# Kernel tuning notes

Hardware: AMD Instinct MI355X
Metric: run time of the kernel (lower is better)

Reference implementation:

```python
import jax, jax.numpy as jnp
import numpy as np

DF = 2  # downsampling_factor

def _conv1x1(x, w, b):
    # x: [N,C,T,H,W], w: [O,C], b: [O]
    return jnp.einsum('ncthw,oc->nothw', x, w) + b[None, :, None, None, None]

def _avgpool(x):
    # AvgPool3d(kernel=(1,k,k), stride=(1,s,s), pad=(0,p,p)), count_include_pad=True
    k, s = DF + 1, DF
    p = (DF + 1) // 2
    summed = jax.lax.reduce_window(
        x, 0.0, jax.lax.add,
        window_dimensions=(1, 1, 1, k, k),
        window_strides=(1, 1, 1, s, s),
        padding=((0, 0), (0, 0), (0, 0), (p, p), (p, p)))
    return summed / float(k * k)

def _grid(T, Hd, Wd, t_scale):
    xg = jnp.arange(Wd, dtype=jnp.float32) / ((Wd - 1) * 0.25) - 2.0
    yg = jnp.arange(Hd, dtype=jnp.float32) / ((Hd - 1) * 0.5) - 1.0
    tg = (jnp.arange(T, dtype=jnp.float32) / ((T - 1) * 0.5) - 1.0) * t_scale
    return jnp.stack(jnp.meshgrid(tg, yg, xg, indexing='ij'), axis=0)  # [3,T,Hd,Wd]

def setup_inputs() -> dict:
    key = jax.random.key(0)
    ks = jax.random.split(key, 9)
    C, IC, OC = 256, 128, 256
    x = jax.random.normal(ks[0], (2, C, 4, 64, 64), dtype=jnp.float32)
    sc = 0.05
    return {
        'x': x,
        'theta_w': jax.random.normal(ks[1], (IC, C), jnp.float32) * sc,
        'theta_b': jax.random.normal(ks[2], (IC,), jnp.float32) * sc,
        'phi_w': jax.random.normal(ks[3], (IC, C), jnp.float32) * sc,
        'phi_b': jax.random.normal(ks[4], (IC,), jnp.float32) * sc,
        'g_w': jax.random.normal(ks[5], (IC, C), jnp.float32) * sc,
        'g_b': jax.random.normal(ks[6], (IC,), jnp.float32) * sc,
        'W_w': jax.random.normal(ks[7], (OC, IC + 3), jnp.float32) * sc,
        'W_b': jax.random.normal(ks[8], (OC,), jnp.float32) * sc,
    }

def reference(x, theta_w, theta_b, phi_w, phi_b, g_w, g_b, W_w, W_b):
    N, C, T, H, W = x.shape
    IC = theta_w.shape[0]
    theta_x = _conv1x1(x, theta_w, theta_b)                       # [N,IC,T,H,W]
    theta_x = theta_x.transpose(0, 2, 3, 4, 1).reshape(N, T * H * W, IC)
    phi_x = _avgpool(_conv1x1(x, phi_w, phi_b))                   # [N,IC,T,Hd,Wd]
    Hd, Wd = phi_x.shape[-2], phi_x.shape[-1]
    phi_x = phi_x.reshape(N, IC, T * Hd * Wd)
    f_x = jax.nn.softmax(jnp.matmul(theta_x, phi_x), axis=-1)     # [N,THW,THdWd]
    g_x = _avgpool(_conv1x1(x, g_w, g_b))                         # [N,IC,T,Hd,Wd]
    grid = _grid(T, Hd, Wd, 0.1)                                   # [3,T,Hd,Wd]
    g_x = jnp.concatenate(
        [g_x, jnp.broadcast_to(grid[None], (N, 3, T, Hd, Wd))], axis=1)
    g_x = g_x.transpose(0, 2, 3, 4, 1).reshape(N, T * Hd * Wd, IC + 3)
    y = jnp.matmul(f_x, g_x)                                       # [N,THW,IC+3]
    y = y.transpose(0, 2, 1).reshape(N, IC + 3, T, H, W)
    return _conv1x1(y, W_w, W_b)
```

## Files before the change

### kernel.cpp

```cpp
#include <hip/hip_runtime.h>
#include <stdint.h>

typedef short short8 __attribute__((ext_vector_type(8)));
typedef float floatx4 __attribute__((ext_vector_type(4)));
typedef float floatx16 __attribute__((ext_vector_type(16)));
typedef unsigned uint4v __attribute__((ext_vector_type(4)));

#define MFMA16(a, b, c) __builtin_amdgcn_mfma_f32_16x16x32_bf16((a), (b), (c), 0, 0, 0)
#define MFMA32(a, b, c) __builtin_amdgcn_mfma_f32_32x32x16_bf16((a), (b), (c), 0, 0, 0)

__device__ __forceinline__ unsigned short f2bf(float f) {
    union { float f; unsigned u; } v; v.f = f;
    unsigned u = v.u;
    unsigned r = (u + 0x7FFFu + ((u >> 16) & 1u)) >> 16;
    return (unsigned short)r;
}
__device__ __forceinline__ unsigned pkfast(float lo, float hi) {
    unsigned a = __float_as_uint(lo) + 0x8000u;
    unsigned b = __float_as_uint(hi) + 0x8000u;
    return __builtin_amdgcn_perm(b, a, 0x07060302u);
}

__global__ void k_prep(const float* th, const float* ph, const float* gw, const float* Ww,
                       unsigned short* TW, unsigned short* PW, unsigned short* GW,
                       unsigned short* Wp) {
    int i = blockIdx.x * 256 + threadIdx.x;
    if (i < 32768) {
        TW[i] = f2bf(th[i]);
    } else if (i < 65536) {
        PW[i - 32768] = f2bf(ph[i - 32768]);
    } else if (i < 98304) {
        GW[i - 65536] = f2bf(gw[i - 65536]);
    } else if (i < 98304 + 256 * 160) {
        int j = i - 98304;
        int oc = j / 160, k = j - oc * 160;
        Wp[j] = (k < 131) ? f2bf(Ww[oc * 131 + k]) : (unsigned short)0;
    }
}

__global__ void k_pool(const float* __restrict__ x, float* __restrict__ xp) {
    int e = blockIdx.x * 256 + threadIdx.x;
    int wd = e & 31, hd = (e >> 5) & 31, t = (e >> 10) & 3, c = (e >> 12) & 255, n = e >> 20;
    const float* base = x + (((size_t)(n * 256 + c) * 4 + t) << 12);
    int h0 = 2 * hd - 1, w0 = 2 * wd - 1;
    float s = 0.f;
    #pragma unroll
    for (int dh = 0; dh < 3; ++dh) {
        int h = h0 + dh;
        if ((unsigned)h < 64u) {
            const float* row = base + h * 64;
            #pragma unroll
            for (int dw = 0; dw < 3; ++dw) {
                int w = w0 + dw;
                if ((unsigned)w < 64u) s += row[w];
            }
        }
    }
    xp[((size_t)(n * 256 + c) << 12) + (t << 10) + (hd << 5) + wd] = s * (1.f / 9.f);
}

__launch_bounds__(256)
__global__ void k_convq(const float* __restrict__ x, const unsigned short* __restrict__ TW,
                        const float* __restrict__ tb, unsigned short* __restrict__ Q) {
    int tid = threadIdx.x, wid = tid >> 6, lane = tid & 63, quad = lane >> 4, l16 = lane & 15;
    int n = blockIdx.y;
    int px = blockIdx.x * 64 + wid * 16 + l16;
    const float* xb = x + ((size_t)n << 22) + px;
    floatx4 acc[8];
    #pragma unroll
    for (int i = 0; i < 8; ++i) acc[i] = (floatx4)0.f;
    for (int kc = 0; kc < 8; ++kc) {
        int cbase = kc * 32 + quad * 8;
        short8 b;
        #pragma unroll
        for (int j = 0; j < 8; ++j) b[j] = (short)f2bf(xb[(size_t)(cbase + j) << 14]);
        #pragma unroll
        for (int mt = 0; mt < 8; ++mt) {
            short8 a = *(const short8*)(TW + (mt * 16 + l16) * 256 + cbase);
            acc[mt] = MFMA16(a, b, acc[mt]);
        }
    }
    unsigned short* Qr = Q + ((((size_t)n << 14) + px) << 7);
    #pragma unroll
    for (int mt = 0; mt < 8; ++mt)
        #pragma unroll
        for (int r = 0; r < 4; ++r) {
            int ic = mt * 16 + quad * 4 + r;
            Qr[ic] = f2bf(acc[mt][r] + tb[ic]);
        }
}

__launch_bounds__(256)
__global__ void k_convkv(const float* __restrict__ xp,
                         const unsigned short* __restrict__ PW, const float* __restrict__ pb,
                         const unsigned short* __restrict__ GW, const float* __restrict__ gb,
                         unsigned short* __restrict__ K, unsigned short* __restrict__ Vt) {
    int tid = threadIdx.x, wid = tid >> 6, lane = tid & 63, quad = lane >> 4, l16 = lane & 15;
    int n = blockIdx.y;
    int k0 = blockIdx.x * 64;
    int key = k0 + wid * 16 + l16;
    const float* xb = xp + ((size_t)n << 20) + key;
    floatx4 ka[8], va[8];
    #pragma unroll
    for (int i = 0; i < 8; ++i) { ka[i] = (floatx4)0.f; va[i] = (floatx4)0.f; }
    for (int kc = 0; kc < 8; ++kc) {
        int cbase = kc * 32 + quad * 8;
        short8 b;
        #pragma unroll
        for (int j = 0; j < 8; ++j) b[j] = (short)f2bf(xb[(size_t)(cbase + j) << 12]);
        #pragma unroll
        for (int mt = 0; mt < 8; ++mt) {
            short8 ap = *(const short8*)(PW + (mt * 16 + l16) * 256 + cbase);
            ka[mt] = MFMA16(ap, b, ka[mt]);
            short8 ag = *(const short8*)(GW + (mt * 16 + l16) * 256 + cbase);
            va[mt] = MFMA16(ag, b, va[mt]);
        }
    }
    int hd = (key >> 5) & 31, wdd = key & 31;
    float frac = ((hd == 0) ? 2.f : 3.f) * ((wdd == 0) ? 2.f : 3.f) * (1.f / 9.f);
    unsigned short* Kr = K + ((((size_t)n << 12) + key) << 7);
    #pragma unroll
    for (int mt = 0; mt < 8; ++mt)
        #pragma unroll
        for (int r = 0; r < 4; ++r) {
            int ic = mt * 16 + quad * 4 + r;
            Kr[ic] = f2bf(ka[mt][r] + pb[ic] * frac);
            Vt[(((size_t)n * 160 + ic) << 12) + key] = f2bf(va[mt][r] + gb[ic] * frac);
        }
    #pragma unroll
    for (int it = 0; it < 8; ++it) {
        int e = it * 256 + tid;
        int row = 128 + (e >> 6);
        int kk = k0 + (e & 63);
        int t = kk >> 10, hh = (kk >> 5) & 31, ww = kk & 31;
        unsigned short v = 0;
        if (row == 128) v = f2bf(((float)t * (1.f / 1.5f) - 1.f) * 0.1f);
        else if (row == 129) v = f2bf((float)hh * (1.f / 15.5f) - 1.f);
        else if (row == 130) v = f2bf((float)ww * (1.f / 7.75f) - 2.f);
        Vt[(((size_t)n * 160 + row) << 12) + kk] = v;
    }
}

__launch_bounds__(256, 2)
__global__ void k_attn(const unsigned short* __restrict__ Q, const unsigned short* __restrict__ K,
                       const unsigned short* __restrict__ Vt, unsigned short* __restrict__ Y,
                       float* __restrict__ L) {
    __shared__ short Klds[64][136];
    __shared__ short Vlds[160][72];
    int tid = threadIdx.x, wid = tid >> 6, lane = tid & 63;
    int l32 = lane & 31, half = lane >> 5;
    int n = blockIdx.y, sp = blockIdx.z;
    int q0 = blockIdx.x * 128 + wid * 32;

    const unsigned short* Qr = Q + ((((size_t)n << 14) + q0 + l32) << 7);
    short8 qf[8];
    #pragma unroll
    for (int kc = 0; kc < 8; ++kc) qf[kc] = *(const short8*)(Qr + kc * 16 + half * 8);

    floatx16 O[5];
    #pragma unroll
    for (int t = 0; t < 5; ++t) O[t] = (floatx16)0.f;
    float lacc = 0.f;

    int krow = tid >> 4, kcol = (tid & 15) * 8;
    int vrow = tid >> 3, vcol = (tid & 7) * 8;
    const unsigned short* kptr = K + ((((size_t)n << 12) + sp * 2048 + krow) << 7) + kcol;
    const unsigned short* vptr = Vt + ((size_t)(n * 160 + vrow) << 12) + sp * 2048 + vcol;

    short8 kpre[4], vpre[5];
    #pragma unroll
    for (int i = 0; i < 4; ++i) kpre[i] = *(const short8*)(kptr + (size_t)i * 16 * 128);
    #pragma unroll
    for (int i = 0; i < 5; ++i) vpre[i] = *(const short8*)(vptr + ((size_t)i * 32 << 12));

    for (int it = 0; it < 32; ++it) {
        __syncthreads();
        #pragma unroll
        for (int i = 0; i < 4; ++i) *(short8*)&Klds[i * 16 + krow][kcol] = kpre[i];
        #pragma unroll
        for (int i = 0; i < 5; ++i) *(short8*)&Vlds[i * 32 + vrow][vcol] = vpre[i];
        __syncthreads();
        if (it < 31) {
            const unsigned short* kp = kptr + (size_t)(it + 1) * 64 * 128;
            const unsigned short* vp = vptr + (size_t)(it + 1) * 64;
            #pragma unroll
            for (int i = 0; i < 4; ++i) kpre[i] = *(const short8*)(kp + (size_t)i * 16 * 128);
            #pragma unroll
            for (int i = 0; i < 5; ++i) vpre[i] = *(const short8*)(vp + ((size_t)i * 32 << 12));
        }

        #pragma unroll
        for (int ks = 0; ks < 2; ++ks) {
            floatx16 st = (floatx16)0.f;
            #pragma unroll
            for (int kc = 0; kc < 8; ++kc) {
                short8 kf = *(const short8*)&Klds[ks * 32 + l32][kc * 16 + half * 8];
                st = MFMA32(kf, qf[kc], st);
            }
            unsigned u[8];
            #pragma unroll
            for (int a = 0; a < 4; ++a) {
                float p0 = exp2f(fmaf(st[4 * a + 0], 1.44269504f, -17.3123404907f));
                float p1 = exp2f(fmaf(st[4 * a + 1], 1.44269504f, -17.3123404907f));
                float p2 = exp2f(fmaf(st[4 * a + 2], 1.44269504f, -17.3123404907f));
                float p3 = exp2f(fmaf(st[4 * a + 3], 1.44269504f, -17.3123404907f));
                lacc += (p0 + p1) + (p2 + p3);
                u[2 * a] = pkfast(p0, p1);
                u[2 * a + 1] = pkfast(p2, p3);
            }
            unsigned xu[8];
            #pragma unroll
            for (int g = 0; g < 8; ++g) xu[g] = (unsigned)__shfl_xor((int)u[g], 32);
            uint4v pw0, pw1;
            pw0[0] = half ? xu[2] : u[0];
            pw0[1] = half ? xu[3] : u[1];
            pw0[2] = half ? u[2] : xu[0];
            pw0[3] = half ? u[3] : xu[1];
            pw1[0] = half ? xu[6] : u[4];
            pw1[1] = half ? xu[7] : u[5];
            pw1[2] = half ? u[6] : xu[4];
            pw1[3] = half ? u[7] : xu[5];
            short8 pf0 = __builtin_bit_cast(short8, pw0);
            short8 pf1 = __builtin_bit_cast(short8, pw1);
            #pragma unroll
            for (int vt = 0; vt < 5; ++vt) {
                short8 vf0 = *(const short8*)&Vlds[vt * 32 + l32][ks * 32 + half * 8];
                O[vt] = MFMA32(vf0, pf0, O[vt]);
                short8 vf1 = *(const short8*)&Vlds[vt * 32 + l32][ks * 32 + 16 + half * 8];
                O[vt] = MFMA32(vf1, pf1, O[vt]);
            }
        }
    }
    float lt = lacc + __shfl_xor(lacc, 32);
    unsigned short* Yb = Y + ((((size_t)(sp * 2 + n) << 14) + q0 + l32) * 160);
    #pragma unroll
    for (int vt = 0; vt < 5; ++vt)
        #pragma unroll
        for (int g = 0; g < 4; ++g) {
            int vd = vt * 32 + 8 * g + 4 * half;
            uint2 w;
            w.x = pkfast(O[vt][4 * g], O[vt][4 * g + 1]);
            w.y = pkfast(O[vt][4 * g + 2], O[vt][4 * g + 3]);
            *(uint2*)(Yb + vd) = w;
        }
    if (lane < 32) L[(((size_t)(sp * 2 + n)) << 14) + q0 + lane] = lt;
}

__launch_bounds__(256)
__global__ void k_convf(const unsigned short* __restrict__ Y, const float* __restrict__ L,
                        const unsigned short* __restrict__ Wp, const float* __restrict__ Wb,
                        float* __restrict__ out) {
    int tid = threadIdx.x, wid = tid >> 6, lane = tid & 63, quad = lane >> 4, l16 = lane & 15;
    int n = blockIdx.y;
    int p0 = blockIdx.x * 64;
    floatx4 acc[4][4];
    #pragma unroll
    for (int i = 0; i < 4; ++i)
        #pragma unroll
        for (int j = 0; j < 4; ++j) acc[i][j] = (floatx4)0.f;
    for (int kc = 0; kc < 5; ++kc) {
        int cb = kc * 32 + quad * 8;
        short8 a[4];
        #pragma unroll
        for (int mt = 0; mt < 4; ++mt)
            a[mt] = *(const short8*)(Wp + (size_t)(wid * 64 + mt * 16 + l16) * 160 + cb);
        #pragma unroll
        for (int sp = 0; sp < 2; ++sp) {
            const unsigned short* Yb = Y + ((((size_t)(sp * 2 + n)) << 14) + p0) * 160;
            #pragma unroll
            for (int nt = 0; nt < 4; ++nt) {
                short8 b = *(const short8*)(Yb + (size_t)(nt * 16 + l16) * 160 + cb);
                #pragma unroll
                for (int mt = 0; mt < 4; ++mt) acc[mt][nt] = MFMA16(a[mt], b, acc[mt][nt]);
            }
        }
    }
    float linv[4];
    #pragma unroll
    for (int nt = 0; nt < 4; ++nt) {
        int p = p0 + nt * 16 + l16;
        linv[nt] = 1.f / (L[(((size_t)n) << 14) + p] + L[(((size_t)(2 + n)) << 14) + p]);
    }
    #pragma unroll
    for (int mt = 0; mt < 4; ++mt)
        #pragma unroll
        for (int r = 0; r < 4; ++r) {
            int oc = wid * 64 + mt * 16 + quad * 4 + r;
            float bb = Wb[oc];
            float* orow = out + ((((size_t)n << 8) + oc) << 14) + p0;
            #pragma unroll
            for (int nt = 0; nt < 4; ++nt)
                orow[nt * 16 + l16] = acc[mt][nt][r] * linv[nt] + bb;
        }
}

extern "C" void kernel_launch(void* const* d_in, const int* in_sizes, int n_in,
                              void* d_out, int out_size, void* d_ws, size_t ws_size,
                              hipStream_t stream) {
    (void)in_sizes; (void)n_in; (void)out_size; (void)ws_size;
    const float* x   = (const float*)d_in[0];
    const float* thw = (const float*)d_in[1];
    const float* thb = (const float*)d_in[2];
    const float* phw = (const float*)d_in[3];
    const float* phb = (const float*)d_in[4];
    const float* gw_ = (const float*)d_in[5];
    const float* gb_ = (const float*)d_in[6];
    const float* Ww  = (const float*)d_in[7];
    const float* Wb  = (const float*)d_in[8];
    float* out = (float*)d_out;

    char* ws = (char*)d_ws;
    size_t off = 0;
    auto alloc = [&](size_t b) { size_t o = off; off += (b + 255) & ~(size_t)255; return o; };
    unsigned short* TW = (unsigned short*)(ws + alloc(32768 * 2));
    unsigned short* PW = (unsigned short*)(ws + alloc(32768 * 2));
    unsigned short* GW = (unsigned short*)(ws + alloc(32768 * 2));
    unsigned short* Wp = (unsigned short*)(ws + alloc(40960 * 2));
    unsigned short* Qb = (unsigned short*)(ws + alloc((size_t)32768 * 128 * 2));
    unsigned short* Kb = (unsigned short*)(ws + alloc((size_t)8192 * 128 * 2));
    unsigned short* Vt = (unsigned short*)(ws + alloc((size_t)2 * 160 * 4096 * 2));
    float*          Lb = (float*)(ws + alloc((size_t)2 * 2 * 16384 * 4));
    unsigned short* Yb = (unsigned short*)(ws + alloc((size_t)2 * 2 * 16384 * 160 * 2));
    float*          xp = (float*)((char*)Yb + (size_t)2 * 16384 * 160 * 2);

    k_prep<<<(139264 + 255) / 256, 256, 0, stream>>>(thw, phw, gw_, Ww, TW, PW, GW, Wp);
    k_pool<<<8192, 256, 0, stream>>>(x, xp);
    k_convq<<<dim3(256, 2), 256, 0, stream>>>(x, TW, thb, Qb);
    k_convkv<<<dim3(64, 2), 256, 0, stream>>>(xp, PW, phb, GW, gb_, Kb, Vt);
    k_attn<<<dim3(128, 2, 2), 256, 0, stream>>>(Qb, Kb, Vt, Yb, Lb);
    k_convf<<<dim3(256, 2), 256, 0, stream>>>(Yb, Lb, Wp, Wb, out);
}
```

Measured before the change: 273.1 us.

## Split attention keys three ways and stage conv outputs through LDS for coalesced stores

The attention kernel now splits the key range into three chunks instead of two, which launches more blocks, and raises the launch-bounds occupancy hint to 3 blocks per SM. The final conv sums over all splits. The Q, K and Vt conv kernels now stage their bf16 results in shared memory and write them out as wide vector stores instead of scattered 16-bit stores. They also use a packed fast bf16 conversion instead of per-element rounding. The extra split adds Y partial traffic, and the higher occupancy target can force register spills in the attention kernel.

```diff
diff --git a/kernel.cpp b/kernel.cpp
--- a/kernel.cpp
+++ b/kernel.cpp
@@ -8,6 +8,8 @@
 
 #define MFMA16(a, b, c) __builtin_amdgcn_mfma_f32_16x16x32_bf16((a), (b), (c), 0, 0, 0)
 #define MFMA32(a, b, c) __builtin_amdgcn_mfma_f32_32x32x16_bf16((a), (b), (c), 0, 0, 0)
+
+#define SPLITS 3
 
 __device__ __forceinline__ unsigned short f2bf(float f) {
     union { float f; unsigned u; } v; v.f = f;
@@ -62,32 +64,42 @@
 __launch_bounds__(256)
 __global__ void k_convq(const float* __restrict__ x, const unsigned short* __restrict__ TW,
                         const float* __restrict__ tb, unsigned short* __restrict__ Q) {
+    __shared__ unsigned short Qs[4][16][132];
     int tid = threadIdx.x, wid = tid >> 6, lane = tid & 63, quad = lane >> 4, l16 = lane & 15;
     int n = blockIdx.y;
-    int px = blockIdx.x * 64 + wid * 16 + l16;
-    const float* xb = x + ((size_t)n << 22) + px;
+    int px0 = blockIdx.x * 64 + wid * 16;
+    const float* xb = x + ((size_t)n << 22) + px0 + l16;
     floatx4 acc[8];
     #pragma unroll
     for (int i = 0; i < 8; ++i) acc[i] = (floatx4)0.f;
     for (int kc = 0; kc < 8; ++kc) {
         int cbase = kc * 32 + quad * 8;
-        short8 b;
-        #pragma unroll
-        for (int j = 0; j < 8; ++j) b[j] = (short)f2bf(xb[(size_t)(cbase + j) << 14]);
+        uint4v bu;
+        #pragma unroll
+        for (int j = 0; j < 4; ++j)
+            bu[j] = pkfast(xb[(size_t)(cbase + 2 * j) << 14],
+                           xb[(size_t)(cbase + 2 * j + 1) << 14]);
+        short8 b = __builtin_bit_cast(short8, bu);
         #pragma unroll
         for (int mt = 0; mt < 8; ++mt) {
             short8 a = *(const short8*)(TW + (mt * 16 + l16) * 256 + cbase);
             acc[mt] = MFMA16(a, b, acc[mt]);
         }
     }
-    unsigned short* Qr = Q + ((((size_t)n << 14) + px) << 7);
-    #pragma unroll
-    for (int mt = 0; mt < 8; ++mt)
-        #pragma unroll
-        for (int r = 0; r < 4; ++r) {
-            int ic = mt * 16 + quad * 4 + r;
-            Qr[ic] = f2bf(acc[mt][r] + tb[ic]);
-        }
+    #pragma unroll
+    for (int mt = 0; mt < 8; ++mt) {
+        int ic = mt * 16 + quad * 4;
+        uint2 w;
+        w.x = pkfast(acc[mt][0] + tb[ic], acc[mt][1] + tb[ic + 1]);
+        w.y = pkfast(acc[mt][2] + tb[ic + 2], acc[mt][3] + tb[ic + 3]);
+        *(uint2*)&Qs[wid][l16][ic] = w;
+    }
+    #pragma unroll
+    for (int i = 0; i < 4; ++i) {
+        int pxl = i * 4 + quad;
+        short8 row = *(const short8*)&Qs[wid][pxl][l16 * 8];
+        *(short8*)(Q + ((((size_t)n << 14) + px0 + pxl) << 7) + l16 * 8) = row;
+    }
 }
 
 __launch_bounds__(256)
@@ -95,6 +107,7 @@
                          const unsigned short* __restrict__ PW, const float* __restrict__ pb,
                          const unsigned short* __restrict__ GW, const float* __restrict__ gb,
                          unsigned short* __restrict__ K, unsigned short* __restrict__ Vt) {
+    __shared__ unsigned short Sh[8576];
     int tid = threadIdx.x, wid = tid >> 6, lane = tid & 63, quad = lane >> 4, l16 = lane & 15;
     int n = blockIdx.y;
     int k0 = blockIdx.x * 64;
@@ -105,9 +118,12 @@
     for (int i = 0; i < 8; ++i) { ka[i] = (floatx4)0.f; va[i] = (floatx4)0.f; }
     for (int kc = 0; kc < 8; ++kc) {
         int cbase = kc * 32 + quad * 8;
-        short8 b;
-        #pragma unroll
-        for (int j = 0; j < 8; ++j) b[j] = (short)f2bf(xb[(size_t)(cbase + j) << 12]);
+        uint4v bu;
+        #pragma unroll
+        for (int j = 0; j < 4; ++j)
+            bu[j] = pkfast(xb[(size_t)(cbase + 2 * j) << 12],
+                           xb[(size_t)(cbase + 2 * j + 1) << 12]);
+        short8 b = __builtin_bit_cast(short8, bu);
         #pragma unroll
         for (int mt = 0; mt < 8; ++mt) {
             short8 ap = *(const short8*)(PW + (mt * 16 + l16) * 256 + cbase);
@@ -118,15 +134,48 @@
     }
     int hd = (key >> 5) & 31, wdd = key & 31;
     float frac = ((hd == 0) ? 2.f : 3.f) * ((wdd == 0) ? 2.f : 3.f) * (1.f / 9.f);
-    unsigned short* Kr = K + ((((size_t)n << 12) + key) << 7);
-    #pragma unroll
-    for (int mt = 0; mt < 8; ++mt)
-        #pragma unroll
-        for (int r = 0; r < 4; ++r) {
-            int ic = mt * 16 + quad * 4 + r;
-            Kr[ic] = f2bf(ka[mt][r] + pb[ic] * frac);
-            Vt[(((size_t)n * 160 + ic) << 12) + key] = f2bf(va[mt][r] + gb[ic] * frac);
-        }
+
+    unsigned short (*Ks)[132] = (unsigned short(*)[132])(Sh + wid * 2112);
+    #pragma unroll
+    for (int mt = 0; mt < 8; ++mt) {
+        int ic = mt * 16 + quad * 4;
+        uint2 w;
+        w.x = pkfast(ka[mt][0] + pb[ic] * frac, ka[mt][1] + pb[ic + 1] * frac);
+        w.y = pkfast(ka[mt][2] + pb[ic + 2] * frac, ka[mt][3] + pb[ic + 3] * frac);
+        *(uint2*)&Ks[l16][ic] = w;
+    }
+    #pragma unroll
+    for (int i = 0; i < 4; ++i) {
+        int pxl = i * 4 + quad;
+        short8 row = *(const short8*)&Ks[pxl][l16 * 8];
+        *(short8*)(K + ((((size_t)n << 12) + k0 + wid * 16 + pxl) << 7) + l16 * 8) = row;
+    }
+
+    __syncthreads();
+    unsigned short (*Vs)[134] = (unsigned short(*)[134])Sh;
+    #pragma unroll
+    for (int mt = 0; mt < 8; ++mt) {
+        int ic = mt * 16 + quad * 4;
+        uint2 w;
+        w.x = pkfast(va[mt][0] + gb[ic] * frac, va[mt][1] + gb[ic + 1] * frac);
+        w.y = pkfast(va[mt][2] + gb[ic + 2] * frac, va[mt][3] + gb[ic + 3] * frac);
+        *(uint2*)&Vs[wid * 16 + l16][ic] = w;
+    }
+    __syncthreads();
+    #pragma unroll
+    for (int it2 = 0; it2 < 4; ++it2) {
+        int ic = it2 * 32 + (tid >> 3);
+        int kk = (tid & 7) * 8;
+        uint4v w;
+        #pragma unroll
+        for (int j = 0; j < 4; ++j) {
+            unsigned s0 = Vs[kk + 2 * j][ic];
+            unsigned s1 = Vs[kk + 2 * j + 1][ic];
+            w[j] = s0 | (s1 << 16);
+        }
+        *(uint4v*)(Vt + (((size_t)(n * 160 + ic)) << 12) + k0 + kk) = w;
+    }
+
     #pragma unroll
     for (int it = 0; it < 8; ++it) {
         int e = it * 256 + tid;
@@ -141,7 +190,7 @@
     }
 }
 
-__launch_bounds__(256, 2)
+__launch_bounds__(256, 3)
 __global__ void k_attn(const unsigned short* __restrict__ Q, const unsigned short* __restrict__ K,
                        const unsigned short* __restrict__ Vt, unsigned short* __restrict__ Y,
                        float* __restrict__ L) {
@@ -150,6 +199,8 @@
     int tid = threadIdx.x, wid = tid >> 6, lane = tid & 63;
     int l32 = lane & 31, half = lane >> 5;
     int n = blockIdx.y, sp = blockIdx.z;
+    int c0 = (sp * 64) / SPLITS, c1 = ((sp + 1) * 64) / SPLITS;
+    int nch = c1 - c0;
     int q0 = blockIdx.x * 128 + wid * 32;
 
     const unsigned short* Qr = Q + ((((size_t)n << 14) + q0 + l32) << 7);
@@ -164,8 +215,8 @@
 
     int krow = tid >> 4, kcol = (tid & 15) * 8;
     int vrow = tid >> 3, vcol = (tid & 7) * 8;
-    const unsigned short* kptr = K + ((((size_t)n << 12) + sp * 2048 + krow) << 7) + kcol;
-    const unsigned short* vptr = Vt + ((size_t)(n * 160 + vrow) << 12) + sp * 2048 + vcol;
+    const unsigned short* kptr = K + ((((size_t)n << 12) + c0 * 64 + krow) << 7) + kcol;
+    const unsigned short* vptr = Vt + ((size_t)(n * 160 + vrow) << 12) + c0 * 64 + vcol;
 
     short8 kpre[4], vpre[5];
     #pragma unroll
@@ -173,14 +224,14 @@
     #pragma unroll
     for (int i = 0; i < 5; ++i) vpre[i] = *(const short8*)(vptr + ((size_t)i * 32 << 12));
 
-    for (int it = 0; it < 32; ++it) {
+    for (int it = 0; it < nch; ++it) {
         __syncthreads();
         #pragma unroll
         for (int i = 0; i < 4; ++i) *(short8*)&Klds[i * 16 + krow][kcol] = kpre[i];
         #pragma unroll
         for (int i = 0; i < 5; ++i) *(short8*)&Vlds[i * 32 + vrow][vcol] = vpre[i];
         __syncthreads();
-        if (it < 31) {
+        if (it + 1 < nch) {
             const unsigned short* kp = kptr + (size_t)(it + 1) * 64 * 128;
             const unsigned short* vp = vptr + (size_t)(it + 1) * 64;
             #pragma unroll
@@ -232,7 +283,8 @@
         }
     }
     float lt = lacc + __shfl_xor(lacc, 32);
-    unsigned short* Yb = Y + ((((size_t)(sp * 2 + n) << 14) + q0 + l32) * 160);
+    int slab = sp * 2 + n;
+    unsigned short* Yb = Y + ((((size_t)slab << 14) + q0 + l32) * 160);
     #pragma unroll
     for (int vt = 0; vt < 5; ++vt)
         #pragma unroll
@@ -243,7 +295,7 @@
             w.y = pkfast(O[vt][4 * g + 2], O[vt][4 * g + 3]);
             *(uint2*)(Yb + vd) = w;
         }
-    if (lane < 32) L[(((size_t)(sp * 2 + n)) << 14) + q0 + lane] = lt;
+    if (lane < 32) L[(((size_t)slab) << 14) + q0 + lane] = lt;
 }
 
 __launch_bounds__(256)
@@ -265,7 +317,7 @@
         for (int mt = 0; mt < 4; ++mt)
             a[mt] = *(const short8*)(Wp + (size_t)(wid * 64 + mt * 16 + l16) * 160 + cb);
         #pragma unroll
-        for (int sp = 0; sp < 2; ++sp) {
+        for (int sp = 0; sp < SPLITS; ++sp) {
             const unsigned short* Yb = Y + ((((size_t)(sp * 2 + n)) << 14) + p0) * 160;
             #pragma unroll
             for (int nt = 0; nt < 4; ++nt) {
@@ -279,7 +331,10 @@
     #pragma unroll
     for (int nt = 0; nt < 4; ++nt) {
         int p = p0 + nt * 16 + l16;
-        linv[nt] = 1.f / (L[(((size_t)n) << 14) + p] + L[(((size_t)(2 + n)) << 14) + p]);
+        float ls = 0.f;
+        #pragma unroll
+        for (int sp = 0; sp < SPLITS; ++sp) ls += L[(((size_t)(sp * 2 + n)) << 14) + p];
+        linv[nt] = 1.f / ls;
     }
     #pragma unroll
     for (int mt = 0; mt < 4; ++mt)
@@ -319,14 +374,15 @@
     unsigned short* Qb = (unsigned short*)(ws + alloc((size_t)32768 * 128 * 2));
     unsigned short* Kb = (unsigned short*)(ws + alloc((size_t)8192 * 128 * 2));
     unsigned short* Vt = (unsigned short*)(ws + alloc((size_t)2 * 160 * 4096 * 2));
-    float*          Lb = (float*)(ws + alloc((size_t)2 * 2 * 16384 * 4));
-    unsigned short* Yb = (unsigned short*)(ws + alloc((size_t)2 * 2 * 16384 * 160 * 2));
-    float*          xp = (float*)((char*)Yb + (size_t)2 * 16384 * 160 * 2);
+    float*          Lb = (float*)(ws + alloc((size_t)SPLITS * 2 * 16384 * 4));
+    size_t ybytes = (size_t)SPLITS * 2 * 16384 * 160 * 2;
+    unsigned short* Yb = (unsigned short*)(ws + alloc(ybytes));
+    float*          xp = (float*)((char*)Yb + (ybytes - (size_t)2 * 256 * 4096 * 4));
 
     k_prep<<<(139264 + 255) / 256, 256, 0, stream>>>(thw, phw, gw_, Ww, TW, PW, GW, Wp);
     k_pool<<<8192, 256, 0, stream>>>(x, xp);
     k_convq<<<dim3(256, 2), 256, 0, stream>>>(x, TW, thb, Qb);
     k_convkv<<<dim3(64, 2), 256, 0, stream>>>(xp, PW, phb, GW, gb_, Kb, Vt);
-    k_attn<<<dim3(128, 2, 2), 256, 0, stream>>>(Qb, Kb, Vt, Yb, Lb);
+    k_attn<<<dim3(128, 2, SPLITS), 256, 0, stream>>>(Qb, Kb, Vt, Yb, Lb);
     k_convf<<<dim3(256, 2), 256, 0, stream>>>(Yb, Lb, Wp, Wb, out);
 }
```

After: 309.4 us. 13.3% more time.
